# Kernel optimization log

Hardware: AMD Instinct MI355X
Metric: run time of the kernel (lower is better)

Reference implementation:

```python
import jax, jax.numpy as jnp
import numpy as np

N = 4096    # nodes per graph
C = 128     # in_channels == out_channels
HEAD = 1
E = 65536   # edges per graph (avg degree 16)


def setup_inputs() -> dict:
    key = jax.random.key(0)
    ks = jax.random.split(key, 24)
    def w(k, shape):
        return jax.random.normal(k, shape, dtype=jnp.float32) * 0.05
    return {
        "x1": jax.random.normal(ks[0], (N, C), dtype=jnp.float32),
        "x2": jax.random.normal(ks[1], (N, C), dtype=jnp.float32),
        "edge_index1": jax.random.randint(ks[2], (2, E), 0, N),
        "edge_index2": jax.random.randint(ks[3], (2, E), 0, N),
        "wl1_w": w(ks[4], (HEAD * C, C)), "wl1_b": w(ks[5], (HEAD * C,)),
        "wr1_w": w(ks[6], (HEAD * C, C)), "wr1_b": w(ks[7], (HEAD * C,)),
        "al1": w(ks[8], (HEAD, C)), "ar1": w(ks[9], (HEAD, C)),
        "wl2_w": w(ks[10], (HEAD * C, C)), "wl2_b": w(ks[11], (HEAD * C,)),
        "wr2_w": w(ks[12], (HEAD * C, C)), "wr2_b": w(ks[13], (HEAD * C,)),
        "al2": w(ks[14], (HEAD, C)), "ar2": w(ks[15], (HEAD, C)),
        "w1_w": w(ks[16], (C, 2 * C)), "w1_b": w(ks[17], (C,)),
        "w2_w": w(ks[18], (C, 2 * C)), "w2_b": w(ks[19], (C,)),
        "lin_w": w(ks[20], (HEAD * C, C)), "lin_b": w(ks[21], (HEAD * C,)),
    }


def _leaky_relu(x):
    return jnp.where(x > 0, x, 0.2 * x)


def _attention(src, tgt, wl, bl, wr, br, al, ar):
    # alpha_l: (N_src,), alpha_r: (N_tot,) -> dense (N_src, N_tot) softmax
    a_l = ((src @ wl.T + bl).reshape(-1, HEAD, C) * al[None]).sum(-1).mean(1)
    a_r = ((tgt @ wr.T + br).reshape(-1, HEAD, C) * ar[None]).sum(-1).mean(1)
    return jax.nn.softmax(_leaky_relu(a_l[:, None] + a_r[None, :]), axis=1)


def _aggr_update(x_i, tgt_all, ei, wl, bl, wr, br, al, ar, ww, wb):
    att = _attention(x_i, tgt_all, wl, bl, wr, br, al, ar)   # (N_i, N_tot)
    ot = x_i - att @ tgt_all                                  # (N_i, C)
    feat = jnp.concatenate([x_i, ot], axis=1)                 # (N_i, 2C)
    n = x_i.shape[0]
    loops = jnp.arange(n)                                     # add_self_loops
    src = jnp.concatenate([ei[0], loops])
    dst = jnp.concatenate([ei[1], loops])
    sums = jax.ops.segment_sum(feat[dst], src, num_segments=n)
    cnt = jax.ops.segment_sum(jnp.ones((src.shape[0],), feat.dtype), src, num_segments=n)
    aggr = sums / cnt[:, None]                                # scatter 'mean'
    return jax.nn.relu(aggr) @ ww.T + wb


def reference(x1, x2, edge_index1, edge_index2,
              wl1_w, wl1_b, wr1_w, wr1_b, al1, ar1,
              wl2_w, wl2_b, wr2_w, wr2_b, al2, ar2,
              w1_w, w1_b, w2_w, w2_b, lin_w, lin_b):
    Xs = [x1, x2]
    eis = [edge_index1, edge_index2]
    layers = [(wl1_w, wl1_b, wr1_w, wr1_b, al1, ar1, w1_w, w1_b),
              (wl2_w, wl2_b, wr2_w, wr2_b, al2, ar2, w2_w, w2_b)]
    for (wl, bl, wr, br, al, ar, ww, wb) in layers:
        tgt = jnp.concatenate(Xs, axis=0)
        Xs = [_aggr_update(Xs[i], tgt, eis[i], wl, bl, wr, br, al, ar, ww, wb)
              for i in range(2)]
    feats = jnp.concatenate(Xs, axis=0) @ lin_w.T + lin_b     # (2N, C)
    return jax.nn.sigmoid(feats @ feats.T)                    # (2N, 2N)
```

## Files before the change

### kernel.cpp

```cpp
#include <hip/hip_runtime.h>
#include <hip/hip_bf16.h>

#define NT 8192
#define NN 4096
#define CD 128
#define NE 65536

typedef __attribute__((ext_vector_type(8))) short bf16x8;
typedef __attribute__((ext_vector_type(16))) float f32x16;
typedef __attribute__((ext_vector_type(4))) float f32x4;

__global__ __launch_bounds__(256) void k_prep(
    const float* __restrict__ W1, const float* __restrict__ W2, const float* __restrict__ WL,
    float* __restrict__ WT1, float* __restrict__ WT2, float* __restrict__ WTL,
    const float* __restrict__ wlw0, const float* __restrict__ wlb0,
    const float* __restrict__ wrw0, const float* __restrict__ wrb0,
    const float* __restrict__ al0, const float* __restrict__ ar0,
    const float* __restrict__ wlw1, const float* __restrict__ wlb1,
    const float* __restrict__ wrw1, const float* __restrict__ wrb1,
    const float* __restrict__ al1, const float* __restrict__ ar1,
    float* __restrict__ VP, int* __restrict__ DEG) {
  int b = blockIdx.x, tid = threadIdx.x;
  if (b < 320) {
    int idx = b * 256 + tid;
    if (idx < 32768) { int c = idx >> 8, k = idx & 255; WT1[k * 128 + c] = W1[idx]; }
    else if (idx < 65536) { int j = idx - 32768; int c = j >> 8, k = j & 255; WT2[k * 128 + c] = W2[j]; }
    else { int j = idx - 65536; int c = j >> 7, k = j & 127; WTL[k * 128 + c] = WL[j]; }
  } else if (b < 322) {
    int L = b - 320;
    const float* wlw = L ? wlw1 : wlw0;
    const float* wlb = L ? wlb1 : wlb0;
    const float* wrw = L ? wrw1 : wrw0;
    const float* wrb = L ? wrb1 : wrb0;
    const float* alv = L ? al1 : al0;
    const float* arv = L ? ar1 : ar0;
    float* vp = VP + L * 258;
    if (tid < 128) {
      int c = tid;
      float sl = 0.f, sr = 0.f;
      for (int h = 0; h < 128; ++h) {
        sl += wlw[h * 128 + c] * alv[h];
        sr += wrw[h * 128 + c] * arv[h];
      }
      vp[c] = sl;
      vp[128 + c] = sr;
      if (c < 2) {
        const float* bb = c ? wrb : wlb;
        const float* aa = c ? arv : alv;
        float s = 0.f;
        for (int h = 0; h < 128; ++h) s += bb[h] * aa[h];
        vp[256 + c] = s;
      }
    }
  } else {
    int idx = (b - 322) * 256 + tid;
    DEG[idx] = 0;
  }
}

__global__ void k_deg(const int* __restrict__ EI1, const int* __restrict__ EI2,
                      int* __restrict__ DEG) {
  int idx = blockIdx.x * 256 + threadIdx.x;
  int g = idx >> 16, e = idx & 65535;
  const int* src = g ? EI2 : EI1;
  atomicAdd(&DEG[g * NN + src[e]], 1);
}

__global__ void k_scanoff(const int* __restrict__ DEG, int* __restrict__ OFFS,
                          int* __restrict__ CURS) {
  int g = blockIdx.x, tid = threadIdx.x;
  __shared__ int part[256];
  int loc[16];
  int s = 0;
  #pragma unroll
  for (int i = 0; i < 16; ++i) { loc[i] = s; s += DEG[g * NN + tid * 16 + i]; }
  part[tid] = s;
  __syncthreads();
  for (int d = 1; d < 256; d <<= 1) {
    int v = part[tid];
    int o = (tid >= d) ? part[tid - d] : 0;
    __syncthreads();
    part[tid] = v + o;
    __syncthreads();
  }
  int excl = tid ? part[tid - 1] : 0;
  #pragma unroll
  for (int i = 0; i < 16; ++i) {
    int o = excl + loc[i];
    OFFS[g * (NN + 1) + tid * 16 + i] = o;
    CURS[g * NN + tid * 16 + i] = o;
  }
  if (tid == 255) OFFS[g * (NN + 1) + NN] = part[255];
}

__global__ void k_fill(const int* __restrict__ EI1, const int* __restrict__ EI2,
                       int* __restrict__ CURS, int* __restrict__ ADJ) {
  int idx = blockIdx.x * 256 + threadIdx.x;
  int g = idx >> 16, e = idx & 65535;
  const int* ei = g ? EI2 : EI1;
  int s = ei[e], d = ei[NE + e];
  int pos = atomicAdd(&CURS[g * NN + s], 1);
  ADJ[g * NE + pos] = d;
}

__global__ void k_alar(const float* __restrict__ X, const float* __restrict__ VP,
                       float* __restrict__ AL, float* __restrict__ AR,
                       int* __restrict__ RANK) {
  if (blockIdx.x < 32) RANK[blockIdx.x * 256 + threadIdx.x] = 0;
  int lane = threadIdx.x & 63;
  int row = blockIdx.x * 4 + (threadIdx.x >> 6);
  float x0 = X[row * 128 + lane], x1 = X[row * 128 + 64 + lane];
  float sl = x0 * VP[lane] + x1 * VP[64 + lane];
  float sr = x0 * VP[128 + lane] + x1 * VP[192 + lane];
  #pragma unroll
  for (int m = 1; m < 64; m <<= 1) {
    sl += __shfl_xor(sl, m, 64);
    sr += __shfl_xor(sr, m, 64);
  }
  if (lane == 0) { AL[row] = sl + VP[256]; AR[row] = sr + VP[257]; }
}

__global__ void k_rank(const float* __restrict__ AR, int* __restrict__ RANK) {
  __shared__ float tile[1024];
  int j = blockIdx.x * 256 + threadIdx.x;
  int base = blockIdx.y * 1024;
  for (int t = threadIdx.x; t < 1024; t += 256) tile[t] = AR[base + t];
  __syncthreads();
  float aj = AR[j];
  int cnt = 0;
  #pragma unroll 8
  for (int u = 0; u < 1024; ++u) {
    float a2 = tile[u];
    cnt += (a2 < aj || (a2 == aj && (base + u) < j)) ? 1 : 0;
  }
  atomicAdd(&RANK[j], cnt);
}

__global__ void k_perm(const int* __restrict__ RANK, const float* __restrict__ AR,
                       int* __restrict__ PERM, float* __restrict__ ARS) {
  int j = blockIdx.x * 256 + threadIdx.x;
  int r = RANK[j];
  PERM[r] = j;
  ARS[r] = AR[j];
}

__global__ __launch_bounds__(256) void k_scanA(
    const float* __restrict__ X, const int* __restrict__ PERM,
    const float* __restrict__ ARS,
    float* __restrict__ P1, float* __restrict__ P2,
    float* __restrict__ CT1, float* __restrict__ CT2,
    float* __restrict__ Q1L, float* __restrict__ Q2L,
    float* __restrict__ QCT1, float* __restrict__ QCT2) {
  __shared__ int pc[64];
  __shared__ float w[2][64];
  __shared__ float part[2][4][32];
  __shared__ float qpart[2][4];
  int b = blockIdx.x;
  int chunk = b >> 2, sub = b & 3;
  int tid = threadIdx.x;
  int a = tid >> 7;
  int g = (tid >> 5) & 3;
  int cl = tid & 31;
  int c = sub * 32 + cl;
  if (tid < 64) {
    int r = chunk * 64 + tid;
    pc[tid] = PERM[r];
    float ar = ARS[r];
    w[0][tid] = __expf(ar);
    w[1][tid] = __expf(0.2f * ar);
  }
  __syncthreads();
  int t0 = g * 16;
  float loc[16];
  float acc = 0.f;
  #pragma unroll 4
  for (int t = 0; t < 16; ++t) {
    acc += w[a][t0 + t] * X[pc[t0 + t] * 128 + c];
    loc[t] = acc;
  }
  part[a][g][cl] = acc;
  float qloc[16];
  float qacc = 0.f;
  bool doQ = (sub == 0 && cl == 0);
  if (doQ) {
    for (int t = 0; t < 16; ++t) { qacc += w[a][t0 + t]; qloc[t] = qacc; }
    qpart[a][g] = qacc;
  }
  __syncthreads();
  float off = (g > 0 ? part[a][0][cl] : 0.f) + (g > 1 ? part[a][1][cl] : 0.f) +
              (g > 2 ? part[a][2][cl] : 0.f);
  float* P = a ? P2 : P1;
  #pragma unroll 4
  for (int t = 0; t < 16; ++t) P[(chunk * 64 + t0 + t) * 128 + c] = loc[t] + off;
  if (g == 3) (a ? CT2 : CT1)[chunk * 128 + c] = off + acc;
  if (doQ) {
    float qoff = (g > 0 ? qpart[a][0] : 0.f) + (g > 1 ? qpart[a][1] : 0.f) +
                 (g > 2 ? qpart[a][2] : 0.f);
    float* Q = a ? Q2L : Q1L;
    for (int t = 0; t < 16; ++t) Q[chunk * 64 + t0 + t] = qloc[t] + qoff;
    if (g == 3) (a ? QCT2 : QCT1)[chunk] = qoff + qacc;
  }
}

__global__ __launch_bounds__(320) void k_scanB(
    const float* __restrict__ CT1, const float* __restrict__ CT2,
    const float* __restrict__ QCT1, const float* __restrict__ QCT2,
    float* __restrict__ OFF1, float* __restrict__ OFF2,
    float* __restrict__ QOF1, float* __restrict__ QOF2) {
  int tid = threadIdx.x;
  if (tid < 128) {
    float acc = 0.f;
    #pragma unroll 8
    for (int ch = 0; ch < 128; ++ch) { acc += CT1[ch * 128 + tid]; OFF1[ch * 128 + tid] = acc; }
  } else if (tid < 256) {
    int c = tid - 128;
    float acc = 0.f;
    #pragma unroll 8
    for (int ch = 0; ch < 128; ++ch) { acc += CT2[ch * 128 + c]; OFF2[ch * 128 + c] = acc; }
  } else if (tid == 256) {
    float acc = 0.f;
    for (int ch = 0; ch < 128; ++ch) { acc += QCT1[ch]; QOF1[ch] = acc; }
  } else if (tid == 257) {
    float acc = 0.f;
    for (int ch = 0; ch < 128; ++ch) { acc += QCT2[ch]; QOF2[ch] = acc; }
  }
}

__global__ void k_combine(const float* __restrict__ X, const float* __restrict__ AL,
                          const float* __restrict__ ARS,
                          const float* __restrict__ P1, const float* __restrict__ P2,
                          const float* __restrict__ OFF1, const float* __restrict__ OFF2,
                          const float* __restrict__ Q1L, const float* __restrict__ Q2L,
                          const float* __restrict__ QOF1, const float* __restrict__ QOF2,
                          float* __restrict__ OT) {
  int row = blockIdx.x * 2 + (threadIdx.x >> 7);
  int c = threadIdx.x & 127;
  float ali = AL[row];
  float A1 = __expf(ali), A2 = __expf(0.2f * ali);
  float xv = -ali;
  int lo = 0, hi = NT;
  while (lo < hi) {
    int mid = (lo + hi) >> 1;
    if (ARS[mid] <= xv) lo = mid + 1; else hi = mid;
  }
  int b = lo - 1;
  float p1 = 0.f, p2 = 0.f, q1 = 0.f, q2 = 0.f;
  if (b >= 0) {
    int ch = b >> 6;
    p1 = P1[b * 128 + c] + (ch ? OFF1[(ch - 1) * 128 + c] : 0.f);
    p2 = P2[b * 128 + c] + (ch ? OFF2[(ch - 1) * 128 + c] : 0.f);
    q1 = Q1L[b] + (ch ? QOF1[ch - 1] : 0.f);
    q2 = Q2L[b] + (ch ? QOF2[ch - 1] : 0.f);
  }
  float T1 = OFF1[127 * 128 + c];
  float QT1 = QOF1[127];
  float num = A1 * (T1 - p1) + A2 * p2;
  float den = A1 * (QT1 - q1) + A2 * q2;
  OT[row * 128 + c] = X[row * 128 + c] - num / den;
}

__global__ __launch_bounds__(256) void k_aggr(const float* __restrict__ X,
                                              const float* __restrict__ OT,
                                              const int* __restrict__ OFFS,
                                              const int* __restrict__ ADJ,
                                              float* __restrict__ AGGR) {
  int node = blockIdx.x * 4 + (threadIdx.x >> 6);
  int lane = threadIdx.x & 63;
  int g = node >> 12, n = node & (NN - 1);
  const int* off = OFFS + g * (NN + 1);
  const int* adj = ADJ + g * NE;
  int beg = off[n], end = off[n + 1];
  const f32x4* src = (const f32x4*)((lane < 32 ? X : OT) + (size_t)g * NN * CD);
  int c4 = lane & 31;
  f32x4 acc = src[n * 32 + c4];
  for (int e = beg; e < end; ++e) {
    int d = adj[e];
    acc += src[d * 32 + c4];
  }
  f32x4 r = acc / (float)(end - beg + 1);
  ((f32x4*)AGGR)[(size_t)node * 64 + (lane < 32 ? c4 : 32 + c4)] = r;
}

template <int KD, bool RELU, bool OBF>
__global__ __launch_bounds__(128) void k_gemm(const float* __restrict__ A,
                                              const float* __restrict__ WT,
                                              const float* __restrict__ bias,
                                              void* __restrict__ out) {
  __shared__ float sA[8 * KD];
  int c = threadIdx.x;
  int r0 = blockIdx.x * 8;
  for (int i = c; i < 8 * KD; i += 128) {
    float a = A[(size_t)r0 * KD + i];
    if (RELU) a = fmaxf(a, 0.f);
    sA[i] = a;
  }
  __syncthreads();
  float acc[8];
  float bc = bias[c];
  #pragma unroll
  for (int i = 0; i < 8; ++i) acc[i] = bc;
  for (int k = 0; k < KD; ++k) {
    float wv = WT[k * 128 + c];
    #pragma unroll
    for (int i = 0; i < 8; ++i) acc[i] += sA[i * KD + k] * wv;
  }
  if (OBF) {
    __hip_bfloat16* o = (__hip_bfloat16*)out;
    #pragma unroll
    for (int i = 0; i < 8; ++i) o[(r0 + i) * 128 + c] = __float2bfloat16(acc[i]);
  } else {
    float* o = (float*)out;
    #pragma unroll
    for (int i = 0; i < 8; ++i) o[(r0 + i) * 128 + c] = acc[i];
  }
}

__device__ inline f32x16 zero16() {
  f32x16 v;
  #pragma unroll
  for (int i = 0; i < 16; ++i) v[i] = 0.f;
  return v;
}

__device__ inline void store_frag(float* __restrict__ out, const f32x16& a,
                                  int grow0, int gcol) {
  #pragma unroll
  for (int r = 0; r < 16; ++r) {
    int rloc = (r & 3) + 8 * (r >> 2);
    float v = a[r];
    out[(size_t)(grow0 + rloc) * 8192 + gcol] =
        __builtin_amdgcn_rcpf(1.f + __expf(-v));
  }
}

__global__ __launch_bounds__(256) void k_final(const unsigned short* __restrict__ F,
                                               float* __restrict__ out) {
  __shared__ unsigned short AT[128 * 128];
  __shared__ unsigned short BT[128 * 128];
  int cb = blockIdx.x, rb = blockIdx.y;
  int tid = threadIdx.x;
  #pragma unroll
  for (int q = 0; q < 8; ++q) {
    int idx = q * 256 + tid;
    int r = idx >> 4, ck = idx & 15;
    unsigned off = (unsigned)((r * 256 + ck * 16) ^ ((r & 7) << 4));
    uint4 va = *(const uint4*)(F + (size_t)(rb * 128 + r) * 128 + ck * 8);
    *(uint4*)((char*)AT + off) = va;
    uint4 vb = *(const uint4*)(F + (size_t)(cb * 128 + r) * 128 + ck * 8);
    *(uint4*)((char*)BT + off) = vb;
  }
  __syncthreads();
  int lane = tid & 63, w = tid >> 6;
  int wr = w >> 1, wc = w & 1;
  int l31 = lane & 31, kh = lane >> 5;
  int xorm = (l31 & 7) << 4;
  int rowA0 = wr * 64 + l31, rowA1 = rowA0 + 32;
  int rowB0 = wc * 64 + l31, rowB1 = rowB0 + 32;
  f32x16 a00 = zero16(), a01 = zero16(), a10 = zero16(), a11 = zero16();
  #pragma unroll
  for (int ks = 0; ks < 8; ++ks) {
    int kb = ks * 32 + kh * 16;
    bf16x8 av0 = *(const bf16x8*)((const char*)AT + ((rowA0 * 256 + kb) ^ xorm));
    bf16x8 av1 = *(const bf16x8*)((const char*)AT + ((rowA1 * 256 + kb) ^ xorm));
    bf16x8 bv0 = *(const bf16x8*)((const char*)BT + ((rowB0 * 256 + kb) ^ xorm));
    bf16x8 bv1 = *(const bf16x8*)((const char*)BT + ((rowB1 * 256 + kb) ^ xorm));
    a00 = __builtin_amdgcn_mfma_f32_32x32x16_bf16(av0, bv0, a00, 0, 0, 0);
    a01 = __builtin_amdgcn_mfma_f32_32x32x16_bf16(av0, bv1, a01, 0, 0, 0);
    a10 = __builtin_amdgcn_mfma_f32_32x32x16_bf16(av1, bv0, a10, 0, 0, 0);
    a11 = __builtin_amdgcn_mfma_f32_32x32x16_bf16(av1, bv1, a11, 0, 0, 0);
  }
  int grow = rb * 128 + wr * 64 + 4 * kh;
  int gcol = cb * 128 + wc * 64 + l31;
  store_frag(out, a00, grow, gcol);
  store_frag(out, a01, grow, gcol + 32);
  store_frag(out, a10, grow + 32, gcol);
  store_frag(out, a11, grow + 32, gcol + 32);
}

extern "C" void kernel_launch(void* const* d_in, const int* in_sizes, int n_in,
                              void* d_out, int out_size, void* d_ws, size_t ws_size,
                              hipStream_t stream) {
  (void)in_sizes; (void)n_in; (void)out_size; (void)ws_size;
  const float* x1 = (const float*)d_in[0];
  const float* x2 = (const float*)d_in[1];
  const int* ei1 = (const int*)d_in[2];
  const int* ei2 = (const int*)d_in[3];
  const float* wl_w[2] = {(const float*)d_in[4], (const float*)d_in[10]};
  const float* wl_b[2] = {(const float*)d_in[5], (const float*)d_in[11]};
  const float* wr_w[2] = {(const float*)d_in[6], (const float*)d_in[12]};
  const float* wr_b[2] = {(const float*)d_in[7], (const float*)d_in[13]};
  const float* alv[2] = {(const float*)d_in[8], (const float*)d_in[14]};
  const float* arv[2] = {(const float*)d_in[9], (const float*)d_in[15]};
  const float* ww_w[2] = {(const float*)d_in[16], (const float*)d_in[18]};
  const float* ww_b[2] = {(const float*)d_in[17], (const float*)d_in[19]};
  const float* lin_w = (const float*)d_in[20];
  const float* lin_b = (const float*)d_in[21];

  char* wp = (char*)d_ws;
  auto alloc = [&](size_t b) -> char* {
    char* p = wp;
    wp += (b + 255) & ~(size_t)255;
    return p;
  };
  float* XA = (float*)alloc((size_t)NT * CD * 4);
  float* XB = (float*)alloc((size_t)NT * CD * 4);
  float* OT = (float*)alloc((size_t)NT * CD * 4);
  float* P1 = (float*)alloc((size_t)NT * CD * 4);
  float* P2 = (float*)alloc((size_t)NT * CD * 4);
  float* AGGR = P1;
  float* CT1 = (float*)alloc(128 * 128 * 4);
  float* CT2 = (float*)alloc(128 * 128 * 4);
  float* OFF1 = (float*)alloc(128 * 128 * 4);
  float* OFF2 = (float*)alloc(128 * 128 * 4);
  float* AL = (float*)alloc(NT * 4);
  float* AR_ = (float*)alloc(NT * 4);
  float* ARS = (float*)alloc(NT * 4);
  float* Q1L = (float*)alloc(NT * 4);
  float* Q2L = (float*)alloc(NT * 4);
  float* QCT1 = (float*)alloc(128 * 4);
  float* QCT2 = (float*)alloc(128 * 4);
  float* QOF1 = (float*)alloc(128 * 4);
  float* QOF2 = (float*)alloc(128 * 4);
  float* VP = (float*)alloc(2 * 258 * 4);
  float* WT1 = (float*)alloc(256 * 128 * 4);
  float* WT2 = (float*)alloc(256 * 128 * 4);
  float* WTL = (float*)alloc(128 * 128 * 4);
  int* RANK = (int*)alloc(NT * 4);
  int* PERM = (int*)alloc(NT * 4);
  int* DEG = (int*)alloc(2 * NN * 4);
  int* OFFS = (int*)alloc(2 * (NN + 1) * 4);
  int* CURS = (int*)alloc(2 * NN * 4);
  int* ADJ = (int*)alloc(2 * NE * 4);
  __hip_bfloat16* FBF = (__hip_bfloat16*)OT;

  hipMemcpyAsync(XA, x1, (size_t)NN * CD * 4, hipMemcpyDeviceToDevice, stream);
  hipMemcpyAsync(XA + (size_t)NN * CD, x2, (size_t)NN * CD * 4, hipMemcpyDeviceToDevice, stream);
  k_prep<<<354, 256, 0, stream>>>(ww_w[0], ww_w[1], lin_w, WT1, WT2, WTL,
                                  wl_w[0], wl_b[0], wr_w[0], wr_b[0], alv[0], arv[0],
                                  wl_w[1], wl_b[1], wr_w[1], wr_b[1], alv[1], arv[1],
                                  VP, DEG);
  k_deg<<<512, 256, 0, stream>>>(ei1, ei2, DEG);
  k_scanoff<<<2, 256, 0, stream>>>(DEG, OFFS, CURS);
  k_fill<<<512, 256, 0, stream>>>(ei1, ei2, CURS, ADJ);

  float* X = XA;
  float* XN = XB;
  for (int L = 0; L < 2; ++L) {
    k_alar<<<2048, 256, 0, stream>>>(X, VP + L * 258, AL, AR_, RANK);
    k_rank<<<dim3(32, 8), 256, 0, stream>>>(AR_, RANK);
    k_perm<<<32, 256, 0, stream>>>(RANK, AR_, PERM, ARS);
    k_scanA<<<512, 256, 0, stream>>>(X, PERM, ARS, P1, P2, CT1, CT2, Q1L, Q2L, QCT1, QCT2);
    k_scanB<<<1, 320, 0, stream>>>(CT1, CT2, QCT1, QCT2, OFF1, OFF2, QOF1, QOF2);
    k_combine<<<4096, 256, 0, stream>>>(X, AL, ARS, P1, P2, OFF1, OFF2, Q1L, Q2L, QOF1, QOF2, OT);
    k_aggr<<<2048, 256, 0, stream>>>(X, OT, OFFS, ADJ, AGGR);
    k_gemm<256, true, false><<<1024, 128, 0, stream>>>(AGGR, L ? WT2 : WT1, ww_b[L], XN);
    float* t = X; X = XN; XN = t;
  }
  k_gemm<128, false, true><<<1024, 128, 0, stream>>>(X, WTL, lin_b, FBF);
  k_final<<<dim3(64, 64), 256, 0, stream>>>((const unsigned short*)FBF, (float*)d_out);
}
```

Before: 319.6 us.

## Fuse setup and per-layer kernels to cut launch count

Folds the input copies into the prep kernel and merges independent setup stages into shared launches: degree count with attention logits, offset scan with rank, CSR fill with permutation. The next layer's attention logits move into the first GEMM's epilogue, and the final linear projection moves into the second GEMM. This removes two memcpys and several small launches, along with the intermediate round-trips for X and the pre-projection features. In exchange, kernels mix heterogeneous block roles, and the GEMM blocks do extra serial work per block.

```diff
diff --git a/kernel.cpp b/kernel.cpp
--- a/kernel.cpp
+++ b/kernel.cpp
@@ -11,6 +11,7 @@
 typedef __attribute__((ext_vector_type(4))) float f32x4;
 
 __global__ __launch_bounds__(256) void k_prep(
+    const float* __restrict__ x1, const float* __restrict__ x2, float* __restrict__ X,
     const float* __restrict__ W1, const float* __restrict__ W2, const float* __restrict__ WL,
     float* __restrict__ WT1, float* __restrict__ WT2, float* __restrict__ WTL,
     const float* __restrict__ wlw0, const float* __restrict__ wlb0,
@@ -21,13 +22,22 @@
     const float* __restrict__ al1, const float* __restrict__ ar1,
     float* __restrict__ VP, int* __restrict__ DEG) {
   int b = blockIdx.x, tid = threadIdx.x;
-  if (b < 320) {
-    int idx = b * 256 + tid;
+  int gid = b * 256 + tid;
+  {
+    const f32x4* s1 = (const f32x4*)x1;
+    const f32x4* s2 = (const f32x4*)x2;
+    f32x4* d = (f32x4*)X;
+    d[gid] = s1[gid];
+    d[gid + NN * CD / 4] = s2[gid];
+  }
+  if (gid < 81920) {
+    int idx = gid;
     if (idx < 32768) { int c = idx >> 8, k = idx & 255; WT1[k * 128 + c] = W1[idx]; }
     else if (idx < 65536) { int j = idx - 32768; int c = j >> 8, k = j & 255; WT2[k * 128 + c] = W2[j]; }
     else { int j = idx - 65536; int c = j >> 7, k = j & 127; WTL[k * 128 + c] = WL[j]; }
-  } else if (b < 322) {
-    int L = b - 320;
+  }
+  if ((b == 508 || b == 509) && tid < 128) {
+    int L = b - 508;
     const float* wlw = L ? wlw1 : wlw0;
     const float* wlb = L ? wlb1 : wlb0;
     const float* wrw = L ? wrw1 : wrw0;
@@ -35,40 +45,59 @@
     const float* alv = L ? al1 : al0;
     const float* arv = L ? ar1 : ar0;
     float* vp = VP + L * 258;
-    if (tid < 128) {
-      int c = tid;
-      float sl = 0.f, sr = 0.f;
-      for (int h = 0; h < 128; ++h) {
-        sl += wlw[h * 128 + c] * alv[h];
-        sr += wrw[h * 128 + c] * arv[h];
-      }
-      vp[c] = sl;
-      vp[128 + c] = sr;
-      if (c < 2) {
-        const float* bb = c ? wrb : wlb;
-        const float* aa = c ? arv : alv;
-        float s = 0.f;
-        for (int h = 0; h < 128; ++h) s += bb[h] * aa[h];
-        vp[256 + c] = s;
-      }
+    int c = tid;
+    float sl = 0.f, sr = 0.f;
+    for (int h = 0; h < 128; ++h) {
+      sl += wlw[h * 128 + c] * alv[h];
+      sr += wrw[h * 128 + c] * arv[h];
     }
-  } else {
-    int idx = (b - 322) * 256 + tid;
-    DEG[idx] = 0;
-  }
-}
-
-__global__ void k_deg(const int* __restrict__ EI1, const int* __restrict__ EI2,
-                      int* __restrict__ DEG) {
-  int idx = blockIdx.x * 256 + threadIdx.x;
-  int g = idx >> 16, e = idx & 65535;
-  const int* src = g ? EI2 : EI1;
-  atomicAdd(&DEG[g * NN + src[e]], 1);
-}
-
-__global__ void k_scanoff(const int* __restrict__ DEG, int* __restrict__ OFFS,
-                          int* __restrict__ CURS) {
-  int g = blockIdx.x, tid = threadIdx.x;
+    vp[c] = sl;
+    vp[128 + c] = sr;
+    if (c < 2) {
+      const float* bb = c ? wrb : wlb;
+      const float* aa = c ? arv : alv;
+      float s = 0.f;
+      for (int h = 0; h < 128; ++h) s += bb[h] * aa[h];
+      vp[256 + c] = s;
+    }
+  }
+  if (gid < 2 * NN) DEG[gid] = 0;
+}
+
+__device__ inline void alar_row(const float* __restrict__ X, const float* __restrict__ VP,
+                                float* __restrict__ AL, float* __restrict__ AR,
+                                int row, int lane) {
+  float x0 = X[row * 128 + lane], x1 = X[row * 128 + 64 + lane];
+  float sl = x0 * VP[lane] + x1 * VP[64 + lane];
+  float sr = x0 * VP[128 + lane] + x1 * VP[192 + lane];
+  #pragma unroll
+  for (int m = 1; m < 64; m <<= 1) {
+    sl += __shfl_xor(sl, m, 64);
+    sr += __shfl_xor(sr, m, 64);
+  }
+  if (lane == 0) { AL[row] = sl + VP[256]; AR[row] = sr + VP[257]; }
+}
+
+__device__ void rank_body(int rb, int tid, const float* __restrict__ AR,
+                          int* __restrict__ RANK) {
+  __shared__ float tile[1024];
+  int jb = rb & 31, tb = rb >> 5;
+  int base = tb * 1024;
+  for (int t = tid; t < 1024; t += 256) tile[t] = AR[base + t];
+  __syncthreads();
+  int j = jb * 256 + tid;
+  float aj = AR[j];
+  int cnt = 0;
+  #pragma unroll 8
+  for (int u = 0; u < 1024; ++u) {
+    float a2 = tile[u];
+    cnt += (a2 < aj || (a2 == aj && (base + u) < j)) ? 1 : 0;
+  }
+  atomicAdd(&RANK[j], cnt);
+}
+
+__device__ void scanoff_body(int g, int tid, const int* __restrict__ DEG,
+                             int* __restrict__ OFFS, int* __restrict__ CURS) {
   __shared__ int part[256];
   int loc[16];
   int s = 0;
@@ -93,49 +122,55 @@
   if (tid == 255) OFFS[g * (NN + 1) + NN] = part[255];
 }
 
-__global__ void k_fill(const int* __restrict__ EI1, const int* __restrict__ EI2,
-                       int* __restrict__ CURS, int* __restrict__ ADJ) {
-  int idx = blockIdx.x * 256 + threadIdx.x;
-  int g = idx >> 16, e = idx & 65535;
-  const int* ei = g ? EI2 : EI1;
-  int s = ei[e], d = ei[NE + e];
-  int pos = atomicAdd(&CURS[g * NN + s], 1);
-  ADJ[g * NE + pos] = d;
-}
-
-__global__ void k_alar(const float* __restrict__ X, const float* __restrict__ VP,
-                       float* __restrict__ AL, float* __restrict__ AR,
-                       int* __restrict__ RANK) {
-  if (blockIdx.x < 32) RANK[blockIdx.x * 256 + threadIdx.x] = 0;
-  int lane = threadIdx.x & 63;
-  int row = blockIdx.x * 4 + (threadIdx.x >> 6);
-  float x0 = X[row * 128 + lane], x1 = X[row * 128 + 64 + lane];
-  float sl = x0 * VP[lane] + x1 * VP[64 + lane];
-  float sr = x0 * VP[128 + lane] + x1 * VP[192 + lane];
-  #pragma unroll
-  for (int m = 1; m < 64; m <<= 1) {
-    sl += __shfl_xor(sl, m, 64);
-    sr += __shfl_xor(sr, m, 64);
-  }
-  if (lane == 0) { AL[row] = sl + VP[256]; AR[row] = sr + VP[257]; }
+__global__ __launch_bounds__(256) void k_s2(
+    const int* __restrict__ EI1, const int* __restrict__ EI2, int* __restrict__ DEG,
+    const float* __restrict__ X, const float* __restrict__ VP0,
+    float* __restrict__ AL, float* __restrict__ AR, int* __restrict__ RANK) {
+  int b = blockIdx.x, tid = threadIdx.x;
+  if (b < 512) {
+    int gid = b * 256 + tid;
+    int g = gid >> 16, e = gid & 65535;
+    const int* src = g ? EI2 : EI1;
+    atomicAdd(&DEG[g * NN + src[e]], 1);
+  } else {
+    int bb = b - 512;
+    if (bb < 32) RANK[bb * 256 + tid] = 0;
+    alar_row(X, VP0, AL, AR, bb * 4 + (tid >> 6), tid & 63);
+  }
+}
+
+__global__ __launch_bounds__(256) void k_s3(
+    const int* __restrict__ DEG, int* __restrict__ OFFS, int* __restrict__ CURS,
+    const float* __restrict__ AR, int* __restrict__ RANK) {
+  int b = blockIdx.x, tid = threadIdx.x;
+  if (b < 2) scanoff_body(b, tid, DEG, OFFS, CURS);
+  else rank_body(b - 2, tid, AR, RANK);
+}
+
+__global__ __launch_bounds__(256) void k_s4(
+    const int* __restrict__ EI1, const int* __restrict__ EI2,
+    int* __restrict__ CURS, int* __restrict__ ADJ,
+    const int* __restrict__ RANK, const float* __restrict__ AR,
+    int* __restrict__ PERM, float* __restrict__ ARS) {
+  int b = blockIdx.x, tid = threadIdx.x;
+  if (b < 512) {
+    int gid = b * 256 + tid;
+    int g = gid >> 16, e = gid & 65535;
+    const int* ei = g ? EI2 : EI1;
+    int s = ei[e], d = ei[NE + e];
+    int pos = atomicAdd(&CURS[g * NN + s], 1);
+    ADJ[g * NE + pos] = d;
+  } else {
+    int j = (b - 512) * 256 + tid;
+    int r = RANK[j];
+    PERM[r] = j;
+    ARS[r] = AR[j];
+  }
 }
 
 __global__ void k_rank(const float* __restrict__ AR, int* __restrict__ RANK) {
-  __shared__ float tile[1024];
-  int j = blockIdx.x * 256 + threadIdx.x;
-  int base = blockIdx.y * 1024;
-  for (int t = threadIdx.x; t < 1024; t += 256) tile[t] = AR[base + t];
-  __syncthreads();
-  float aj = AR[j];
-  int cnt = 0;
-  #pragma unroll 8
-  for (int u = 0; u < 1024; ++u) {
-    float a2 = tile[u];
-    cnt += (a2 < aj || (a2 == aj && (base + u) < j)) ? 1 : 0;
-  }
-  atomicAdd(&RANK[j], cnt);
-}
-
+  rank_body(blockIdx.x, threadIdx.x, AR, RANK);
+}
 __global__ void k_perm(const int* __restrict__ RANK, const float* __restrict__ AR,
                        int* __restrict__ PERM, float* __restrict__ ARS) {
   int j = blockIdx.x * 256 + threadIdx.x;
@@ -146,7 +181,7 @@
 
 __global__ __launch_bounds__(256) void k_scanA(
     const float* __restrict__ X, const int* __restrict__ PERM,
-    const float* __restrict__ ARS,
+    const float* __restrict__ ARS, int* __restrict__ RANK,
     float* __restrict__ P1, float* __restrict__ P2,
     float* __restrict__ CT1, float* __restrict__ CT2,
     float* __restrict__ Q1L, float* __restrict__ Q2L,
@@ -156,6 +191,7 @@
   __shared__ float part[2][4][32];
   __shared__ float qpart[2][4];
   int b = blockIdx.x;
+  if (b < 32) RANK[b * 256 + threadIdx.x] = 0;
   int chunk = b >> 2, sub = b & 3;
   int tid = threadIdx.x;
   int a = tid >> 7;
@@ -281,38 +317,85 @@
   ((f32x4*)AGGR)[(size_t)node * 64 + (lane < 32 ? c4 : 32 + c4)] = r;
 }
 
-template <int KD, bool RELU, bool OBF>
-__global__ __launch_bounds__(128) void k_gemm(const float* __restrict__ A,
-                                              const float* __restrict__ WT,
-                                              const float* __restrict__ bias,
-                                              void* __restrict__ out) {
-  __shared__ float sA[8 * KD];
+__global__ __launch_bounds__(128) void k_gemmA(const float* __restrict__ A,
+                                               const float* __restrict__ WT,
+                                               const float* __restrict__ bias,
+                                               float* __restrict__ XN,
+                                               const float* __restrict__ VP1,
+                                               float* __restrict__ AL,
+                                               float* __restrict__ AR) {
+  __shared__ float sA[8 * 256];
+  __shared__ float sB[8 * 128];
   int c = threadIdx.x;
   int r0 = blockIdx.x * 8;
-  for (int i = c; i < 8 * KD; i += 128) {
-    float a = A[(size_t)r0 * KD + i];
-    if (RELU) a = fmaxf(a, 0.f);
-    sA[i] = a;
-  }
+  for (int i = c; i < 8 * 256; i += 128) sA[i] = fmaxf(A[(size_t)r0 * 256 + i], 0.f);
   __syncthreads();
   float acc[8];
   float bc = bias[c];
   #pragma unroll
   for (int i = 0; i < 8; ++i) acc[i] = bc;
-  for (int k = 0; k < KD; ++k) {
+  for (int k = 0; k < 256; ++k) {
     float wv = WT[k * 128 + c];
     #pragma unroll
-    for (int i = 0; i < 8; ++i) acc[i] += sA[i * KD + k] * wv;
-  }
-  if (OBF) {
-    __hip_bfloat16* o = (__hip_bfloat16*)out;
+    for (int i = 0; i < 8; ++i) acc[i] += sA[i * 256 + k] * wv;
+  }
+  #pragma unroll
+  for (int i = 0; i < 8; ++i) {
+    XN[(r0 + i) * 128 + c] = acc[i];
+    sB[i * 128 + c] = acc[i];
+  }
+  __syncthreads();
+  int lane = threadIdx.x & 63, wv_ = threadIdx.x >> 6;
+  #pragma unroll
+  for (int i = 0; i < 4; ++i) {
+    int row = wv_ * 4 + i;
+    float x0 = sB[row * 128 + lane], x1 = sB[row * 128 + 64 + lane];
+    float sl = x0 * VP1[lane] + x1 * VP1[64 + lane];
+    float sr = x0 * VP1[128 + lane] + x1 * VP1[192 + lane];
     #pragma unroll
-    for (int i = 0; i < 8; ++i) o[(r0 + i) * 128 + c] = __float2bfloat16(acc[i]);
-  } else {
-    float* o = (float*)out;
+    for (int m = 1; m < 64; m <<= 1) {
+      sl += __shfl_xor(sl, m, 64);
+      sr += __shfl_xor(sr, m, 64);
+    }
+    if (lane == 0) { AL[r0 + row] = sl + VP1[256]; AR[r0 + row] = sr + VP1[257]; }
+  }
+}
+
+__global__ __launch_bounds__(128) void k_gemmB(const float* __restrict__ A,
+                                               const float* __restrict__ WT,
+                                               const float* __restrict__ bias,
+                                               const float* __restrict__ WTL,
+                                               const float* __restrict__ LINB,
+                                               __hip_bfloat16* __restrict__ FBF) {
+  __shared__ float sA[8 * 256];
+  __shared__ float sB[8 * 128];
+  int c = threadIdx.x;
+  int r0 = blockIdx.x * 8;
+  for (int i = c; i < 8 * 256; i += 128) sA[i] = fmaxf(A[(size_t)r0 * 256 + i], 0.f);
+  __syncthreads();
+  float acc[8];
+  float bc = bias[c];
+  #pragma unroll
+  for (int i = 0; i < 8; ++i) acc[i] = bc;
+  for (int k = 0; k < 256; ++k) {
+    float wv = WT[k * 128 + c];
     #pragma unroll
-    for (int i = 0; i < 8; ++i) o[(r0 + i) * 128 + c] = acc[i];
-  }
+    for (int i = 0; i < 8; ++i) acc[i] += sA[i * 256 + k] * wv;
+  }
+  #pragma unroll
+  for (int i = 0; i < 8; ++i) sB[i * 128 + c] = acc[i];
+  __syncthreads();
+  float acl[8];
+  float lb = LINB[c];
+  #pragma unroll
+  for (int i = 0; i < 8; ++i) acl[i] = lb;
+  for (int k = 0; k < 128; ++k) {
+    float wl = WTL[k * 128 + c];
+    #pragma unroll
+    for (int i = 0; i < 8; ++i) acl[i] += sB[i * 128 + k] * wl;
+  }
+  #pragma unroll
+  for (int i = 0; i < 8; ++i) FBF[(r0 + i) * 128 + c] = __float2bfloat16(acl[i]);
 }
 
 __device__ inline f32x16 zero16() {
@@ -433,29 +516,24 @@
   int* ADJ = (int*)alloc(2 * NE * 4);
   __hip_bfloat16* FBF = (__hip_bfloat16*)OT;
 
-  hipMemcpyAsync(XA, x1, (size_t)NN * CD * 4, hipMemcpyDeviceToDevice, stream);
-  hipMemcpyAsync(XA + (size_t)NN * CD, x2, (size_t)NN * CD * 4, hipMemcpyDeviceToDevice, stream);
-  k_prep<<<354, 256, 0, stream>>>(ww_w[0], ww_w[1], lin_w, WT1, WT2, WTL,
+  k_prep<<<512, 256, 0, stream>>>(x1, x2, XA, ww_w[0], ww_w[1], lin_w, WT1, WT2, WTL,
                                   wl_w[0], wl_b[0], wr_w[0], wr_b[0], alv[0], arv[0],
                                   wl_w[1], wl_b[1], wr_w[1], wr_b[1], alv[1], arv[1],
                                   VP, DEG);
-  k_deg<<<512, 256, 0, stream>>>(ei1, ei2, DEG);
-  k_scanoff<<<2, 256, 0, stream>>>(DEG, OFFS, CURS);
-  k_fill<<<512, 256, 0, stream>>>(ei1, ei2, CURS, ADJ);
-
-  float* X = XA;
-  float* XN = XB;
-  for (int L = 0; L < 2; ++L) {
-    k_alar<<<2048, 256, 0, stream>>>(X, VP + L * 258, AL, AR_, RANK);
-    k_rank<<<dim3(32, 8), 256, 0, stream>>>(AR_, RANK);
-    k_perm<<<32, 256, 0, stream>>>(RANK, AR_, PERM, ARS);
-    k_scanA<<<512, 256, 0, stream>>>(X, PERM, ARS, P1, P2, CT1, CT2, Q1L, Q2L, QCT1, QCT2);
-    k_scanB<<<1, 320, 0, stream>>>(CT1, CT2, QCT1, QCT2, OFF1, OFF2, QOF1, QOF2);
-    k_combine<<<4096, 256, 0, stream>>>(X, AL, ARS, P1, P2, OFF1, OFF2, Q1L, Q2L, QOF1, QOF2, OT);
-    k_aggr<<<2048, 256, 0, stream>>>(X, OT, OFFS, ADJ, AGGR);
-    k_gemm<256, true, false><<<1024, 128, 0, stream>>>(AGGR, L ? WT2 : WT1, ww_b[L], XN);
-    float* t = X; X = XN; XN = t;
-  }
-  k_gemm<128, false, true><<<1024, 128, 0, stream>>>(X, WTL, lin_b, FBF);
+  k_s2<<<2560, 256, 0, stream>>>(ei1, ei2, DEG, XA, VP, AL, AR_, RANK);
+  k_s3<<<258, 256, 0, stream>>>(DEG, OFFS, CURS, AR_, RANK);
+  k_s4<<<544, 256, 0, stream>>>(ei1, ei2, CURS, ADJ, RANK, AR_, PERM, ARS);
+  k_scanA<<<512, 256, 0, stream>>>(XA, PERM, ARS, RANK, P1, P2, CT1, CT2, Q1L, Q2L, QCT1, QCT2);
+  k_scanB<<<1, 320, 0, stream>>>(CT1, CT2, QCT1, QCT2, OFF1, OFF2, QOF1, QOF2);
+  k_combine<<<4096, 256, 0, stream>>>(XA, AL, ARS, P1, P2, OFF1, OFF2, Q1L, Q2L, QOF1, QOF2, OT);
+  k_aggr<<<2048, 256, 0, stream>>>(XA, OT, OFFS, ADJ, AGGR);
+  k_gemmA<<<1024, 128, 0, stream>>>(AGGR, WT1, ww_b[0], XB, VP + 258, AL, AR_);
+  k_rank<<<256, 256, 0, stream>>>(AR_, RANK);
+  k_perm<<<32, 256, 0, stream>>>(RANK, AR_, PERM, ARS);
+  k_scanA<<<512, 256, 0, stream>>>(XB, PERM, ARS, RANK, P1, P2, CT1, CT2, Q1L, Q2L, QCT1, QCT2);
+  k_scanB<<<1, 320, 0, stream>>>(CT1, CT2, QCT1, QCT2, OFF1, OFF2, QOF1, QOF2);
+  k_combine<<<4096, 256, 0, stream>>>(XB, AL, ARS, P1, P2, OFF1, OFF2, Q1L, Q2L, QOF1, QOF2, OT);
+  k_aggr<<<2048, 256, 0, stream>>>(XB, OT, OFFS, ADJ, AGGR);
+  k_gemmB<<<1024, 128, 0, stream>>>(AGGR, WT2, ww_b[1], WTL, lin_b, FBF);
   k_final<<<dim3(64, 64), 256, 0, stream>>>((const unsigned short*)FBF, (float*)d_out);
 }
```

New measurement: 301.2 us. 1.06x faster.
